# Performance work log

Hardware: AMD Instinct MI355X
Metric: run time of the kernel (lower is better)

The kernel has to match this reference:

```python
import jax, jax.numpy as jnp
import numpy as np

N, D = 12288, 64


def _ggc(x, adj, W, wih, whh, bih, bhh):
    # Gated graph conv, num_layers=1 (PyG semantics):
    #   m = adj @ (x @ W); x' = GRUCell(m, x)
    m = adj @ (x @ W)                      # [N, D]
    gi = m @ wih.T + bih                   # [N, 3D]
    gh = x @ whh.T + bhh                   # [N, 3D]
    i_r, i_z, i_n = jnp.split(gi, 3, axis=-1)
    h_r, h_z, h_n = jnp.split(gh, 3, axis=-1)
    r = jax.nn.sigmoid(i_r + h_r)
    z = jax.nn.sigmoid(i_z + h_z)
    n = jnp.tanh(i_n + r * h_n)
    return (1.0 - z) * n + z * x


def setup_inputs() -> dict:
    key = jax.random.key(0)
    ks = jax.random.split(key, 8)
    s = 1.0 / np.sqrt(D)
    return {
        "x": jax.random.normal(ks[0], (N, D), jnp.float32),
        "adj": jax.random.uniform(ks[1], (N, N), jnp.float32),
        "W1": jax.random.normal(ks[2], (D, D), jnp.float32) * s,
        "wih1": jax.random.normal(ks[3], (3 * D, D), jnp.float32) * s,
        "whh1": jax.random.normal(ks[4], (3 * D, D), jnp.float32) * s,
        "bih1": jnp.zeros((3 * D,), jnp.float32),
        "bhh1": jnp.zeros((3 * D,), jnp.float32),
        "W2": jax.random.normal(ks[5], (D, D), jnp.float32) * s,
        "wih2": jax.random.normal(ks[6], (3 * D, D), jnp.float32) * s,
        "whh2": jax.random.normal(ks[7], (3 * D, D), jnp.float32) * s,
        "bih2": jnp.zeros((3 * D,), jnp.float32),
        "bhh2": jnp.zeros((3 * D,), jnp.float32),
    }


def reference(x, adj, W1, wih1, whh1, bih1, bhh1, W2, wih2, whh2, bih2, bhh2):
    h = jax.nn.relu(_ggc(x, adj, W1, wih1, whh1, bih1, bhh1))
    # dropout is a no-op in eval mode (training=False)
    return jax.nn.relu(_ggc(h, adj, W2, wih2, whh2, bih2, bhh2))
```

## Files before the change

kernel.cpp:

```cpp
#include <hip/hip_runtime.h>
#include <hip/hip_bf16.h>
#include <cstdint>

#define NN 12288

typedef __attribute__((ext_vector_type(8))) short bfrag8;
typedef __attribute__((ext_vector_type(4))) float f32x4;
typedef __attribute__((ext_vector_type(4))) uint16_t u16x4;
typedef __attribute__((ext_vector_type(8))) uint16_t u16x8;

__device__ __forceinline__ uint16_t f2bf_rtn(float f) {
    uint32_t u = __float_as_uint(f);
    return (uint16_t)((u + 0x7fffu + ((u >> 16) & 1u)) >> 16);
}
__device__ __forceinline__ void split_bf(float f, uint16_t& hb, uint16_t& lb) {
    uint32_t u = __float_as_uint(f);
    hb = (uint16_t)(u >> 16);
    float fr = f - __uint_as_float(u & 0xffff0000u);
    lb = f2bf_rtn(fr);
}

__global__ void wt4_kernel(const float* __restrict__ w0, const float* __restrict__ w1,
                           const float* __restrict__ w2, const float* __restrict__ w3,
                           float* __restrict__ o0, float* __restrict__ o1,
                           float* __restrict__ o2, float* __restrict__ o3) {
    const float* w; float* o;
    switch (blockIdx.y) {
        case 0: w = w0; o = o0; break;
        case 1: w = w1; o = o1; break;
        case 2: w = w2; o = o2; break;
        default: w = w3; o = o3; break;
    }
    int i = blockIdx.x * 256 + threadIdx.x;
    if (i < 192 * 64) {
        int r = i / 64, k = i % 64;
        o[k * 192 + r] = w[i];
    }
}

__global__ void __launch_bounds__(256) xw_kernel(const float* __restrict__ X,
                                                 const float* __restrict__ W,
                                                 uint16_t* __restrict__ Bpk) {
    __shared__ __align__(16) float sW[64 * 65];
    __shared__ __align__(16) float sX[64 * 65];
    const int t = threadIdx.x;
    const int rb = blockIdx.x * 64;
    for (int i = t; i < 4096; i += 256) {
        int rr = i >> 6, cc = i & 63;
        sW[rr * 65 + cc] = W[i];
        sX[rr * 65 + cc] = X[(size_t)rb * 64 + i];
    }
    __syncthreads();
    const int r = t & 63;
    const int c0 = (t >> 6) * 16;
    float acc[16];
#pragma unroll
    for (int i = 0; i < 16; i++) acc[i] = 0.f;
    for (int k = 0; k < 64; k++) {
        float xv = sX[r * 65 + k];
#pragma unroll
        for (int i = 0; i < 16; i++) acc[i] += xv * sW[k * 65 + c0 + i];
    }
    const int j = rb + r;
    const size_t base = (size_t)(j >> 6) * 8192 + (size_t)((j >> 3) & 7) * 512 + (j & 7);
#pragma unroll
    for (int i = 0; i < 16; i++) {
        uint16_t hb, lb;
        split_bf(acc[i], hb, lb);
        size_t idx = base + (size_t)(c0 + i) * 8;
        Bpk[idx] = hb;
        Bpk[idx + 4096] = lb;
    }
}

__global__ void __launch_bounds__(256, 2) spmm_kernel(
    const float* __restrict__ adj,
    const uint16_t* __restrict__ Bpk,
    float* __restrict__ partial,
    int ktiles, int rev) {
    __shared__ __align__(16) uint16_t sAhi[64 * 72];
    __shared__ __align__(16) uint16_t sAlo[64 * 72];
    __shared__ __align__(16) uint16_t sB[8192];
    const int t = threadIdx.x;
    const int rb = blockIdx.x;
    const int kc = blockIdx.y;
    const int tile0 = kc * ktiles;
    const int wave = t >> 6, lane = t & 63;

    const int srow16 = t >> 4;
    const int skk = (t & 15) * 4;

    const float* aptr = adj + (size_t)rb * 64 * NN;

    f32x4 acc[4];
#pragma unroll
    for (int i = 0; i < 4; i++) {
        acc[i][0] = 0.f; acc[i][1] = 0.f; acc[i][2] = 0.f; acc[i][3] = 0.f;
    }

    int pt = rev ? (ktiles - 1) : 0;
    f32x4 ld[4];
#pragma unroll
    for (int it = 0; it < 4; ++it) {
        int row = it * 16 + srow16;
        ld[it] = *(const f32x4*)(aptr + (size_t)row * NN + (size_t)(tile0 + pt) * 64 + skk);
    }
    u16x8 bld[4];
    {
        const u16x8* bsrc = (const u16x8*)(Bpk + (size_t)(tile0 + pt) * 8192);
#pragma unroll
        for (int i = 0; i < 4; ++i) bld[i] = bsrc[i * 256 + t];
    }

    const int arow = wave * 16 + (lane & 15);
    const int kq = lane >> 4;

    for (int tl = 0; tl < ktiles; ++tl) {
        __syncthreads();
#pragma unroll
        for (int it = 0; it < 4; ++it) {
            int row = it * 16 + srow16;
            u16x4 hi, lo;
#pragma unroll
            for (int q = 0; q < 4; q++) {
                uint16_t hb, lb;
                split_bf(ld[it][q], hb, lb);
                hi[q] = hb; lo[q] = lb;
            }
            *(u16x4*)&sAhi[row * 72 + skk] = hi;
            *(u16x4*)&sAlo[row * 72 + skk] = lo;
        }
#pragma unroll
        for (int i = 0; i < 4; ++i) ((u16x8*)sB)[i * 256 + t] = bld[i];
        __syncthreads();
        if (tl + 1 < ktiles) {
            int pn = rev ? (ktiles - 2 - tl) : (tl + 1);
#pragma unroll
            for (int it = 0; it < 4; ++it) {
                int row = it * 16 + srow16;
                ld[it] = *(const f32x4*)(aptr + (size_t)row * NN + (size_t)(tile0 + pn) * 64 + skk);
            }
            const u16x8* b2 = (const u16x8*)(Bpk + (size_t)(tile0 + pn) * 8192);
#pragma unroll
            for (int i = 0; i < 4; ++i) bld[i] = b2[i * 256 + t];
        }
#pragma unroll
        for (int ks = 0; ks < 2; ++ks) {
            const int koff = ks * 32 + kq * 8;
            bfrag8 ahi = *(const bfrag8*)&sAhi[arow * 72 + koff];
            bfrag8 alo = *(const bfrag8*)&sAlo[arow * 72 + koff];
            const int bko = ((ks * 4 + kq) * 64) * 8;
#pragma unroll
            for (int ct = 0; ct < 4; ++ct) {
                int col = ct * 16 + (lane & 15);
                bfrag8 bh = *(const bfrag8*)&sB[bko + col * 8];
                bfrag8 bl = *(const bfrag8*)&sB[4096 + bko + col * 8];
                acc[ct] = __builtin_amdgcn_mfma_f32_16x16x32_bf16(ahi, bh, acc[ct], 0, 0, 0);
                acc[ct] = __builtin_amdgcn_mfma_f32_16x16x32_bf16(alo, bh, acc[ct], 0, 0, 0);
                acc[ct] = __builtin_amdgcn_mfma_f32_16x16x32_bf16(ahi, bl, acc[ct], 0, 0, 0);
            }
        }
    }
    float* pout = partial + (size_t)kc * ((size_t)NN * 64);
    const int orow = rb * 64 + wave * 16 + (lane >> 4) * 4;
    const int ocol = lane & 15;
#pragma unroll
    for (int ct = 0; ct < 4; ++ct) {
#pragma unroll
        for (int r = 0; r < 4; ++r) {
            pout[(size_t)(orow + r) * 64 + ct * 16 + ocol] = acc[ct][r];
        }
    }
}

__global__ void __launch_bounds__(256, 4) gru_kernel(
    const float* __restrict__ partial, int ksplit,
    const float* __restrict__ Xin,
    const float* __restrict__ wtih,
    const float* __restrict__ wthh,
    const float* __restrict__ bih,
    const float* __restrict__ bhh,
    float* __restrict__ hout) {
    __shared__ __align__(16) float sM[32 * 64];
    __shared__ __align__(16) float sX[32 * 64];
    const int t = threadIdx.x;
    const int nb = blockIdx.x * 32;
    for (int e = t; e < 2048; e += 256) {
        size_t gi = (size_t)nb * 64 + e;
        float s = 0.f;
        for (int p = 0; p < ksplit; p++) s += partial[(size_t)p * ((size_t)NN * 64) + gi];
        sM[e] = s;
        sX[e] = Xin[gi];
    }
    __syncthreads();
    const int wave = t >> 6, lane = t & 63;
    const int nodebase = wave * 8;
    float a_ir[8], a_iz[8], a_in[8], a_hr[8], a_hz[8], a_hn[8];
#pragma unroll
    for (int n = 0; n < 8; n++) {
        a_ir[n] = 0.f; a_iz[n] = 0.f; a_in[n] = 0.f;
        a_hr[n] = 0.f; a_hz[n] = 0.f; a_hn[n] = 0.f;
    }
    for (int k = 0; k < 64; k++) {
        float w0 = wtih[k * 192 + lane];
        float w1 = wtih[k * 192 + 64 + lane];
        float w2 = wtih[k * 192 + 128 + lane];
        float w3 = wthh[k * 192 + lane];
        float w4 = wthh[k * 192 + 64 + lane];
        float w5 = wthh[k * 192 + 128 + lane];
#pragma unroll
        for (int n = 0; n < 8; n++) {
            float mv = sM[(nodebase + n) * 64 + k];
            float xv = sX[(nodebase + n) * 64 + k];
            a_ir[n] += w0 * mv; a_iz[n] += w1 * mv; a_in[n] += w2 * mv;
            a_hr[n] += w3 * xv; a_hz[n] += w4 * xv; a_hn[n] += w5 * xv;
        }
    }
    const float b0 = bih[lane], b1 = bih[64 + lane], b2 = bih[128 + lane];
    const float b3 = bhh[lane], b4 = bhh[64 + lane], b5 = bhh[128 + lane];
#pragma unroll
    for (int n = 0; n < 8; n++) {
        float ir = a_ir[n] + b0, iz = a_iz[n] + b1, inn = a_in[n] + b2;
        float hr = a_hr[n] + b3, hz = a_hz[n] + b4, hn = a_hn[n] + b5;
        float r = 1.f / (1.f + __expf(-(ir + hr)));
        float z = 1.f / (1.f + __expf(-(iz + hz)));
        float nt = tanhf(inn + r * hn);
        float xv = sX[(nodebase + n) * 64 + lane];
        float o = (1.f - z) * nt + z * xv;
        o = fmaxf(o, 0.f);
        size_t oi = (size_t)(nb + nodebase + n) * 64 + lane;
        hout[oi] = o;
    }
}

extern "C" void kernel_launch(void* const* d_in, const int* in_sizes, int n_in,
                              void* d_out, int out_size, void* d_ws, size_t ws_size,
                              hipStream_t stream) {
    const float* x    = (const float*)d_in[0];
    const float* adj  = (const float*)d_in[1];
    const float* W1   = (const float*)d_in[2];
    const float* wih1 = (const float*)d_in[3];
    const float* whh1 = (const float*)d_in[4];
    const float* bih1 = (const float*)d_in[5];
    const float* bhh1 = (const float*)d_in[6];
    const float* W2   = (const float*)d_in[7];
    const float* wih2 = (const float*)d_in[8];
    const float* whh2 = (const float*)d_in[9];
    const float* bih2 = (const float*)d_in[10];
    const float* bhh2 = (const float*)d_in[11];
    float* out = (float*)d_out;

    char* p = (char*)d_ws;
    float* wtih1 = (float*)p; p += (size_t)192 * 64 * 4;
    float* wthh1 = (float*)p; p += (size_t)192 * 64 * 4;
    float* wtih2 = (float*)p; p += (size_t)192 * 64 * 4;
    float* wthh2 = (float*)p; p += (size_t)192 * 64 * 4;
    float* h     = (float*)p; p += (size_t)NN * 64 * 4;
    uint16_t* Bpk = (uint16_t*)p; p += (size_t)NN * 64 * 2 * 2;
    float* partial = (float*)p;
    size_t used = (size_t)(p - (char*)d_ws);
    size_t unit = (size_t)NN * 64 * 4;

    int ksplit = 1;
    const int opts[4] = {4, 3, 2, 1};
    for (int i = 0; i < 4; i++) {
        if (used + (size_t)opts[i] * unit <= ws_size) { ksplit = opts[i]; break; }
    }
    int ktiles = 192 / ksplit;

    wt4_kernel<<<dim3(48, 4), 256, 0, stream>>>(wih1, whh1, wih2, whh2,
                                                wtih1, wthh1, wtih2, wthh2);

    xw_kernel<<<192, 256, 0, stream>>>(x, W1, Bpk);
    spmm_kernel<<<dim3(192, ksplit), 256, 0, stream>>>(adj, Bpk, partial, ktiles, 0);
    gru_kernel<<<384, 256, 0, stream>>>(partial, ksplit, x, wtih1, wthh1, bih1, bhh1, h);
    xw_kernel<<<192, 256, 0, stream>>>(h, W2, Bpk);
    spmm_kernel<<<dim3(192, ksplit), 256, 0, stream>>>(adj, Bpk, partial, ktiles, 1);
    gru_kernel<<<384, 256, 0, stream>>>(partial, ksplit, h, wtih2, wthh2, bih2, bhh2, out);
}
```

Before: 370.8 us.

## Double-buffer spmm register prefetch, XOR-swizzle LDS A tiles, raise split-K and occupancy

The spmm kernel now prefetches two K-tiles ahead into alternating register sets so global loads for tile t+2 overlap the compute of tile t. The padded A tile layout in shared memory is replaced by a 128-byte-row XOR swizzle, which shrinks LDS use and is meant to avoid bank conflicts. Launch bounds rise from 2 to 4 blocks per SM, and the split-K options now allow up to 16 splits. The aim is to hide memory latency on the dense adjacency stream, at the cost of more registers per thread, more partial sums for the GRU kernel to reduce, and a loop that assumes an even tile count.

```diff
diff --git a/kernel.cpp b/kernel.cpp
--- a/kernel.cpp
+++ b/kernel.cpp
@@ -18,6 +18,12 @@
     hb = (uint16_t)(u >> 16);
     float fr = f - __uint_as_float(u & 0xffff0000u);
     lb = f2bf_rtn(fr);
+}
+
+__device__ __forceinline__ void lds_sync() {
+    asm volatile("s_waitcnt lgkmcnt(0)" ::: "memory");
+    __builtin_amdgcn_s_barrier();
+    asm volatile("" ::: "memory");
 }
 
 __global__ void wt4_kernel(const float* __restrict__ w0, const float* __restrict__ w1,
@@ -73,24 +79,24 @@
     }
 }
 
-__global__ void __launch_bounds__(256, 2) spmm_kernel(
+__global__ void __launch_bounds__(256, 4) spmm_kernel(
     const float* __restrict__ adj,
     const uint16_t* __restrict__ Bpk,
     float* __restrict__ partial,
     int ktiles, int rev) {
-    __shared__ __align__(16) uint16_t sAhi[64 * 72];
-    __shared__ __align__(16) uint16_t sAlo[64 * 72];
+    __shared__ __align__(16) uint16_t sAhi[4096];
+    __shared__ __align__(16) uint16_t sAlo[4096];
     __shared__ __align__(16) uint16_t sB[8192];
     const int t = threadIdx.x;
     const int rb = blockIdx.x;
     const int kc = blockIdx.y;
     const int tile0 = kc * ktiles;
     const int wave = t >> 6, lane = t & 63;
-
     const int srow16 = t >> 4;
     const int skk = (t & 15) * 4;
-
     const float* aptr = adj + (size_t)rb * 64 * NN;
+    const int arow = wave * 16 + (lane & 15);
+    const int kq = lane >> 4;
 
     f32x4 acc[4];
 #pragma unroll
@@ -98,25 +104,24 @@
         acc[i][0] = 0.f; acc[i][1] = 0.f; acc[i][2] = 0.f; acc[i][3] = 0.f;
     }
 
-    int pt = rev ? (ktiles - 1) : 0;
-    f32x4 ld[4];
-#pragma unroll
-    for (int it = 0; it < 4; ++it) {
-        int row = it * 16 + srow16;
-        ld[it] = *(const f32x4*)(aptr + (size_t)row * NN + (size_t)(tile0 + pt) * 64 + skk);
-    }
-    u16x8 bld[4];
-    {
-        const u16x8* bsrc = (const u16x8*)(Bpk + (size_t)(tile0 + pt) * 8192);
-#pragma unroll
-        for (int i = 0; i < 4; ++i) bld[i] = bsrc[i * 256 + t];
-    }
-
-    const int arow = wave * 16 + (lane & 15);
-    const int kq = lane >> 4;
-
-    for (int tl = 0; tl < ktiles; ++tl) {
-        __syncthreads();
+    f32x4 lA0[4], lA1[4];
+    u16x8 lB0[4], lB1[4];
+
+    auto tid2glob = [&](int i) { return tile0 + (rev ? (ktiles - 1 - i) : i); };
+
+    auto load_tile = [&](int tl, f32x4 (&lA)[4], u16x8 (&lB)[4]) {
+        const float* ap = aptr + (size_t)tid2glob(tl) * 64;
+#pragma unroll
+        for (int it = 0; it < 4; ++it) {
+            int row = it * 16 + srow16;
+            lA[it] = *(const f32x4*)(ap + (size_t)row * NN + skk);
+        }
+        const u16x8* bsrc = (const u16x8*)(Bpk + (size_t)tid2glob(tl) * 8192);
+#pragma unroll
+        for (int i = 0; i < 4; ++i) lB[i] = bsrc[i * 256 + t];
+    };
+
+    auto stage_tile = [&](f32x4 (&lA)[4], u16x8 (&lB)[4]) {
 #pragma unroll
         for (int it = 0; it < 4; ++it) {
             int row = it * 16 + srow16;
@@ -124,32 +129,25 @@
 #pragma unroll
             for (int q = 0; q < 4; q++) {
                 uint16_t hb, lb;
-                split_bf(ld[it][q], hb, lb);
+                split_bf(lA[it][q], hb, lb);
                 hi[q] = hb; lo[q] = lb;
             }
-            *(u16x4*)&sAhi[row * 72 + skk] = hi;
-            *(u16x4*)&sAlo[row * 72 + skk] = lo;
-        }
-#pragma unroll
-        for (int i = 0; i < 4; ++i) ((u16x8*)sB)[i * 256 + t] = bld[i];
-        __syncthreads();
-        if (tl + 1 < ktiles) {
-            int pn = rev ? (ktiles - 2 - tl) : (tl + 1);
-#pragma unroll
-            for (int it = 0; it < 4; ++it) {
-                int row = it * 16 + srow16;
-                ld[it] = *(const f32x4*)(aptr + (size_t)row * NN + (size_t)(tile0 + pn) * 64 + skk);
-            }
-            const u16x8* b2 = (const u16x8*)(Bpk + (size_t)(tile0 + pn) * 8192);
-#pragma unroll
-            for (int i = 0; i < 4; ++i) bld[i] = b2[i * 256 + t];
-        }
+            int off = row * 128 + (((skk >> 3) ^ (row & 7)) << 4) + ((skk & 7) << 1);
+            *(u16x4*)((char*)sAhi + off) = hi;
+            *(u16x4*)((char*)sAlo + off) = lo;
+        }
+#pragma unroll
+        for (int i = 0; i < 4; ++i) ((u16x8*)sB)[i * 256 + t] = lB[i];
+    };
+
+    auto compute_tile = [&]() {
 #pragma unroll
         for (int ks = 0; ks < 2; ++ks) {
-            const int koff = ks * 32 + kq * 8;
-            bfrag8 ahi = *(const bfrag8*)&sAhi[arow * 72 + koff];
-            bfrag8 alo = *(const bfrag8*)&sAlo[arow * 72 + koff];
-            const int bko = ((ks * 4 + kq) * 64) * 8;
+            const int chunk = ks * 4 + kq;
+            const int aoff = arow * 128 + ((chunk ^ (arow & 7)) << 4);
+            bfrag8 ahi = *(const bfrag8*)((const char*)sAhi + aoff);
+            bfrag8 alo = *(const bfrag8*)((const char*)sAlo + aoff);
+            const int bko = chunk * 512;
 #pragma unroll
             for (int ct = 0; ct < 4; ++ct) {
                 int col = ct * 16 + (lane & 15);
@@ -160,7 +158,24 @@
                 acc[ct] = __builtin_amdgcn_mfma_f32_16x16x32_bf16(ahi, bl, acc[ct], 0, 0, 0);
             }
         }
-    }
+    };
+
+    load_tile(0, lA0, lB0);
+    load_tile(1, lA1, lB1);
+
+    for (int tl = 0; tl < ktiles; tl += 2) {
+        lds_sync();
+        stage_tile(lA0, lB0);
+        lds_sync();
+        if (tl + 2 < ktiles) load_tile(tl + 2, lA0, lB0);
+        compute_tile();
+        lds_sync();
+        stage_tile(lA1, lB1);
+        lds_sync();
+        if (tl + 3 < ktiles) load_tile(tl + 3, lA1, lB1);
+        compute_tile();
+    }
+
     float* pout = partial + (size_t)kc * ((size_t)NN * 64);
     const int orow = rb * 64 + wave * 16 + (lane >> 4) * 4;
     const int ocol = lane & 15;
@@ -262,8 +277,8 @@
     size_t unit = (size_t)NN * 64 * 4;
 
     int ksplit = 1;
-    const int opts[4] = {4, 3, 2, 1};
-    for (int i = 0; i < 4; i++) {
+    const int opts[5] = {16, 8, 4, 2, 1};
+    for (int i = 0; i < 5; i++) {
         if (used + (size_t)opts[i] * unit <= ws_size) { ksplit = opts[i]; break; }
     }
     int ktiles = 192 / ksplit;
```

New measurement: 460.0 us. 24.1% more time.
